# Performance work log

Measured on AMD Instinct MI355X. Metric: run time of the kernel, lower is better.

The kernel has to match this reference:

```python
import jax, jax.numpy as jnp
import numpy as np

L, H, D, N, M, P, C, IMG, B = 12, 12, 768, 197, 3072, 16, 3, 224, 16
SKIP_AT = (3, 6, 9, 12)


def pos_emb(n, d):
    i = jnp.arange(n, dtype=jnp.float32)[:, None]
    j = jnp.arange(d)[None, :]
    je = (j // 2) * 2  # j for even, j-1 for odd
    ang = i / jnp.power(10000.0, je.astype(jnp.float32) / d)
    return jnp.where(j % 2 == 0, jnp.sin(ang), jnp.cos(ang))  # [n, d]


def layer_norm(x, g, b):
    mu = x.mean(-1, keepdims=True)
    var = x.var(-1, keepdims=True)
    return (x - mu) / jnp.sqrt(var + 1e-5) * g + b


def setup_inputs() -> dict:
    key = jax.random.key(0)
    ks = jax.random.split(key, 16)
    s = 0.02
    f32 = jnp.float32
    return {
        "images": jax.random.normal(ks[0], (B, C, IMG, IMG), f32),
        "class_token": jax.random.uniform(ks[1], (1, D), f32),
        "Wp": jax.random.normal(ks[2], (D, P * P * C), f32) * s,
        "bp": jnp.zeros((D,), f32),
        "Wq": jax.random.normal(ks[3], (L, H, D, D), f32) * s,
        "bq": jnp.zeros((L, H, D), f32),
        "Wk": jax.random.normal(ks[4], (L, H, D, D), f32) * s,
        "bk": jnp.zeros((L, H, D), f32),
        "Wv": jax.random.normal(ks[5], (L, H, D, D), f32) * s,
        "bv": jnp.zeros((L, H, D), f32),
        "Wm": jax.random.normal(ks[6], (L, N, H * N), f32) * s,
        "bm": jnp.zeros((L, N), f32),
        "g1": jnp.ones((L, D), f32),
        "be1": jnp.zeros((L, D), f32),
        "W1": jax.random.normal(ks[7], (L, M, D), f32) * s,
        "b1": jnp.zeros((L, M), f32),
        "W2": jax.random.normal(ks[8], (L, D, M), f32) * s,
        "b2": jnp.zeros((L, D), f32),
        "g2": jnp.ones((L, D), f32),
        "be2": jnp.zeros((L, D), f32),
    }


def reference(images, class_token, Wp, bp, Wq, bq, Wk, bk, Wv, bv, Wm, bm,
              g1, be1, W1, b1, W2, b2, g2, be2):
    b = images.shape[0]
    Hn, Wn = IMG // P, IMG // P
    # einops 'b c (patch_x h) (patch_y w) -> b (h w) (patch_x patch_y c)'
    x = images.reshape(b, C, P, Hn, P, Wn).transpose(0, 3, 5, 2, 4, 1)
    patches = x.reshape(b, Hn * Wn, P * P * C)
    tokens = patches @ Wp.T + bp  # [b, N-1, D]
    cls = jnp.broadcast_to(class_token[None], (b, 1, D))
    out = jnp.concatenate([cls, tokens], axis=1) + pos_emb(N, D)[None]
    scale = 1.0 / jnp.sqrt(jnp.float32(N - 1))
    skips = []
    for l in range(L):
        x0 = out
        q = jnp.einsum('bnd,hed->bhne', x0, Wq[l]) + bq[l][None, :, None, :]
        k = jnp.einsum('bnd,hed->bhne', x0, Wk[l]) + bk[l][None, :, None, :]
        v = jnp.einsum('bnd,hed->bhne', x0, Wv[l]) + bv[l][None, :, None, :]
        attn = jax.nn.softmax(jnp.einsum('bhne,bhme->bhnm', q, k) * scale, axis=-1)
        o = jnp.einsum('bhnm,bhme->bhne', attn, v).reshape(b, H * N, D)
        # transpose -> [b, D, H*N], Linear(H*N -> N), transpose back
        msa = jnp.einsum('bfd,nf->bnd', o, Wm[l]) + bm[l][None, :, None]
        x1 = layer_norm(x0 + msa, g1[l], be1[l])
        hdn = jax.nn.gelu(x1 @ W1[l].T + b1[l], approximate=False)
        out = layer_norm(x1 + (hdn @ W2[l].T + b2[l]), g2[l], be2[l])
        if l + 1 in SKIP_AT:
            skips.append(out[:, 1:, :])
    return (out[:, 1:, :], *skips)
```

## Files before the change

### kernel.cpp

```cpp
#include <hip/hip_runtime.h>
#include <cstdint>
#include <cstddef>

typedef __bf16 bf16;
typedef __bf16 bf16x8 __attribute__((ext_vector_type(8)));
typedef float f32x4 __attribute__((ext_vector_type(4)));

#define DEVINL __device__ __forceinline__

typedef const __attribute__((address_space(1))) void* as1cv;
typedef __attribute__((address_space(3))) void* as3v;

DEVINL void gload16(const bf16* g, bf16* l) {
    __builtin_amdgcn_global_load_lds((as1cv)g, (as3v)l, 16, 0, 0);
}

static constexpr int Lh = 12, Hh = 12, Dh = 768, Nh = 197, Mh = 3072, Bh = 16;
static constexpr int BN   = Bh * Nh;
static constexpr int NPAT = Bh * 196;
static constexpr int HD   = Hh * Dh;
static constexpr int QKN  = 2 * HD;
static constexpr int QKV3 = 3 * HD;
static constexpr int NP   = 256;
static constexpr int FHN  = Hh * Nh;
static constexpr int FP   = 2368;
static constexpr size_t SEC = (size_t)Bh * 196 * Dh;
static constexpr long LS3 = (long)QKV3 * Dh;
static constexpr long PART = (long)BN * Dh;

template<int AF32, int BF32, int OUTBF, int BIAS, int ACT, int ZFILL>
__global__ __launch_bounds__(256, 3) void gemm_bt(
    const void* __restrict__ Av, long sAy, long sAz, int lda,
    const void* __restrict__ Bv, long sBy, long sBz, int ldb,
    void* __restrict__ Cv, long sCy, long sCz, int ldc,
    const float* __restrict__ bias, long sBiasY,
    int Mv, int Nv, int K, int tilesN, int kChunk)
{
    __shared__ __align__(16) bf16 Asm[128 * 32];
    __shared__ __align__(16) bf16 Bsm[128 * 32];
    const int bx = blockIdx.x;
    const int tm = bx / tilesN, tn = bx % tilesN;
    const long aoff = (long)blockIdx.y * sAy + (long)blockIdx.z * sAz + (long)tm * 128 * lda;
    const long boff = (long)blockIdx.y * sBy + (long)blockIdx.z * sBz + (long)tn * 128 * ldb;
    const int tid = threadIdx.x;
    const int lane = tid & 63, wid = tid >> 6;
    const int ar = tid >> 2, ac = (tid & 3) << 3;
    const bf16* Ag = (const bf16*)Av + aoff + (long)ar * lda + ac;
    const bf16* Bg = (const bf16*)Bv + boff + (long)ar * ldb + ac;
    const float* Af = (const float*)Av + aoff + (long)ar * lda + ac;
    const float* Bf = (const float*)Bv + boff + (long)ar * ldb + ac;
    bf16* lA = Asm + wid * 512;
    bf16* lB = Bsm + wid * 512;
    const int mw = (wid >> 1) * 64, nw = (wid & 1) * 64;
    const int fr = lane & 15, fq = lane >> 4;
    const int kBeg = kChunk ? blockIdx.y * kChunk : 0;
    const int kEnd = kChunk ? min(K, kBeg + kChunk) : K;
    f32x4 acc[4][4] = {};
    for (int k0 = kBeg; k0 < kEnd; k0 += 32) {
        if (AF32) {
            const float* p0 = Af + k0;
            const float* p1 = p0 + (long)64 * lda;
            f32x4 a0 = *(const f32x4*)p0, a1 = *(const f32x4*)(p0 + 4);
            f32x4 a2 = *(const f32x4*)p1, a3 = *(const f32x4*)(p1 + 4);
            bf16x8 r0, r1;
#pragma unroll
            for (int i = 0; i < 4; i++) { r0[i] = (bf16)a0[i]; r0[i + 4] = (bf16)a1[i];
                                          r1[i] = (bf16)a2[i]; r1[i + 4] = (bf16)a3[i]; }
            *(bf16x8*)&Asm[ar * 32 + ac] = r0;
            *(bf16x8*)&Asm[(ar + 64) * 32 + ac] = r1;
        } else {
            gload16(Ag + k0, lA);
            gload16(Ag + (long)64 * lda + k0, lA + 2048);
        }
        if (BF32) {
            const float* p0 = Bf + k0;
            const float* p1 = p0 + (long)64 * ldb;
            f32x4 a0 = *(const f32x4*)p0, a1 = *(const f32x4*)(p0 + 4);
            f32x4 a2 = *(const f32x4*)p1, a3 = *(const f32x4*)(p1 + 4);
            bf16x8 r0, r1;
#pragma unroll
            for (int i = 0; i < 4; i++) { r0[i] = (bf16)a0[i]; r0[i + 4] = (bf16)a1[i];
                                          r1[i] = (bf16)a2[i]; r1[i + 4] = (bf16)a3[i]; }
            *(bf16x8*)&Bsm[ar * 32 + ac] = r0;
            *(bf16x8*)&Bsm[(ar + 64) * 32 + ac] = r1;
        } else {
            gload16(Bg + k0, lB);
            gload16(Bg + (long)64 * ldb + k0, lB + 2048);
        }
        __syncthreads();
        bf16x8 af[4], bv[4];
#pragma unroll
        for (int i = 0; i < 4; i++) af[i] = *(const bf16x8*)&Asm[(mw + i * 16 + fr) * 32 + (fq << 3)];
#pragma unroll
        for (int j = 0; j < 4; j++) bv[j] = *(const bf16x8*)&Bsm[(nw + j * 16 + fr) * 32 + (fq << 3)];
#pragma unroll
        for (int i = 0; i < 4; i++)
#pragma unroll
            for (int j = 0; j < 4; j++)
                acc[i][j] = __builtin_amdgcn_mfma_f32_16x16x32_bf16(af[i], bv[j], acc[i][j], 0, 0, 0);
        __syncthreads();
    }
    const long cb = (long)blockIdx.y * sCy + (long)blockIdx.z * sCz;
    const float* biasp = bias ? bias + (long)blockIdx.y * sBiasY : nullptr;
#pragma unroll
    for (int i = 0; i < 4; i++) {
        const int row0 = tm * 128 + mw + i * 16 + fq * 4;
#pragma unroll
        for (int j = 0; j < 4; j++) {
            const int col = tn * 128 + nw + j * 16 + fr;
            const bool cok = (col < Nv);
            if (!cok && !ZFILL) continue;
            float bc = (BIAS == 1 && cok) ? biasp[col] : 0.f;
#pragma unroll
            for (int r = 0; r < 4; r++) {
                const int rr = row0 + r;
                if (rr >= Mv) continue;
                float v;
                if (cok) {
                    v = acc[i][j][r];
                    if (BIAS == 1) v += bc;
                    if (BIAS == 2) v += biasp[rr];
                    if (ACT) v = 0.5f * v * (1.f + erff(v * 0.70710678118654752f));
                } else v = 0.f;
                const long ci = cb + (long)rr * ldc + col;
                if (OUTBF) ((bf16*)Cv)[ci] = (bf16)v;
                else       ((float*)Cv)[ci] = v;
            }
        }
    }
}

__global__ __launch_bounds__(512, 2) void gemm256(
    const bf16* __restrict__ A, int lda,
    const bf16* __restrict__ B, int ldb,
    bf16* __restrict__ C, int ldc,
    const float* __restrict__ bias,
    int Mv, int K, int tilesN)
{
    __shared__ __align__(16) bf16 As[2][2][8192];
    __shared__ __align__(16) bf16 Bs[2][2][8192];
    const int bx = blockIdx.x;
    const int bm = (bx / tilesN) * 256, bn = (bx % tilesN) * 256;
    const int tid = threadIdx.x;
    const int lane = tid & 63, wid = tid >> 6;
    const int wr = wid >> 2, wc = wid & 3;
    const int fr = lane & 15, fq = lane >> 4;
    const int srow = lane >> 3;
    const int scol = (((lane & 7) ^ srow) << 3);
    const int KT = K >> 6;

    auto STA = [&](int buf, int half, int kt) {
        const bf16* g = A + (size_t)(bm + half * 128) * lda + kt * 64 + scol;
        bf16* l0 = &As[buf][half][0] + wid * 512;
#pragma unroll
        for (int j = 0; j < 2; ++j)
            gload16(g + (size_t)(wid * 8 + j * 64 + srow) * lda, l0 + j * 4096);
    };
    auto STB = [&](int buf, int half, int kt) {
        const bf16* g = B + (size_t)(bn + half * 128) * ldb + kt * 64 + scol;
        bf16* l0 = &Bs[buf][half][0] + wid * 512;
#pragma unroll
        for (int j = 0; j < 2; ++j)
            gload16(g + (size_t)(wid * 8 + j * 64 + srow) * ldb, l0 + j * 4096);
    };

    f32x4 acc[8][4] = {};
    const int swz = (fr & 7) << 3;

    STB(0, 0, 0); STB(0, 1, 0);
    STA(0, 0, 0); STA(0, 1, 0);
    if (KT > 1) { STB(1, 0, 1); STB(1, 1, 1); }
    if (KT > 1) asm volatile("s_waitcnt vmcnt(4)" ::: "memory");
    else        asm volatile("s_waitcnt vmcnt(0)" ::: "memory");
    asm volatile("s_barrier" ::: "memory");

    for (int t = 0; t < KT; ++t) {
        const int d = t & 1;
        bf16x8 bfr[4][2];
#pragma unroll
        for (int q = 0; q < 4; ++q) {
            if (q == 0) {
#pragma unroll
                for (int j = 0; j < 4; ++j)
#pragma unroll
                    for (int ks = 0; ks < 2; ++ks) {
                        const int rl = (wc & 1) * 64 + j * 16 + fr;
                        bfr[j][ks] = *(const bf16x8*)&Bs[d][wc >> 1][rl * 64 + (((ks << 5) | (fq << 3)) ^ swz)];
                    }
            }
            bf16x8 afr[2][2];
#pragma unroll
            for (int ii = 0; ii < 2; ++ii)
#pragma unroll
                for (int ks = 0; ks < 2; ++ks) {
                    const int rl = q * 32 + ii * 16 + fr;
                    afr[ii][ks] = *(const bf16x8*)&As[d][wr][rl * 64 + (((ks << 5) | (fq << 3)) ^ swz)];
                }
            if (q == 0 && t + 1 < KT) STA(d ^ 1, 0, t + 1);
            if (q == 1 && t + 1 < KT) STA(d ^ 1, 1, t + 1);
            if (q == 2 && t + 2 < KT) STB(d, 0, t + 2);
            if (q == 3 && t + 2 < KT) STB(d, 1, t + 2);
            asm volatile("s_barrier" ::: "memory");
            asm volatile("s_waitcnt lgkmcnt(0)" ::: "memory");
            __builtin_amdgcn_s_setprio(1);
#pragma unroll
            for (int ks = 0; ks < 2; ++ks)
#pragma unroll
                for (int ii = 0; ii < 2; ++ii)
#pragma unroll
                    for (int j = 0; j < 4; ++j)
                        acc[(q << 1) | ii][j] =
                            __builtin_amdgcn_mfma_f32_16x16x32_bf16(afr[ii][ks], bfr[j][ks],
                                                                    acc[(q << 1) | ii][j], 0, 0, 0);
            __builtin_amdgcn_s_setprio(0);
            if (q == 3) {
                if (t + 2 < KT) asm volatile("s_waitcnt vmcnt(4)" ::: "memory");
                else            asm volatile("s_waitcnt vmcnt(0)" ::: "memory");
            }
            asm volatile("s_barrier" ::: "memory");
        }
    }

    const int row0c = bm + wr * 128;
    const int col0 = bn + wc * 64;
#pragma unroll
    for (int ri = 0; ri < 8; ++ri)
#pragma unroll
        for (int j = 0; j < 4; ++j) {
            const int col = col0 + j * 16 + fr;
            const float bc = bias[col];
#pragma unroll
            for (int r = 0; r < 4; ++r) {
                const int rr = row0c + ri * 16 + fq * 4 + r;
                if (rr < Mv) C[(size_t)rr * ldc + col] = (bf16)(acc[ri][j][r] + bc);
            }
        }
}

__global__ __launch_bounds__(256) void vtrans_k(const bf16* __restrict__ qkv, bf16* __restrict__ vT) {
    __shared__ bf16 t[64][72];
    const int eb = (blockIdx.x >> 2) << 6;
    const int nb = (blockIdx.x & 3) << 6;
    const int h = blockIdx.y, b = blockIdx.z;
    const int tid = threadIdx.x;
    const int lr = tid >> 2;
    const int lc = (tid & 3) << 4;
    const int n = nb + lr;
    if (n < Nh) {
        const bf16* src = qkv + (size_t)(b * Nh + n) * QKV3 + 2 * HD + h * Dh + eb + lc;
        *(bf16x8*)&t[lr][lc] = *(const bf16x8*)src;
        *(bf16x8*)&t[lr][lc + 8] = *(const bf16x8*)(src + 8);
    } else {
        bf16x8 z = {};
        *(bf16x8*)&t[lr][lc] = z; *(bf16x8*)&t[lr][lc + 8] = z;
    }
    __syncthreads();
    bf16* dst = vT + ((size_t)(b * Hh + h) * Dh + eb + lr) * NP + nb + lc;
    bf16x8 o0, o1;
#pragma unroll
    for (int j = 0; j < 8; j++) { o0[j] = t[lc + j][lr]; o1[j] = t[lc + 8 + j][lr]; }
    *(bf16x8*)dst = o0; *(bf16x8*)(dst + 8) = o1;
}

__global__ __launch_bounds__(256) void cvt_k(const float* __restrict__ in, bf16* __restrict__ out, long n) {
    const long i = ((long)blockIdx.x * 256 + threadIdx.x) * 8;
    if (i >= n) return;
    f32x4 a = *(const f32x4*)(in + i);
    f32x4 b = *(const f32x4*)(in + i + 4);
    bf16x8 r;
#pragma unroll
    for (int j = 0; j < 4; j++) { r[j] = (bf16)a[j]; r[j + 4] = (bf16)b[j]; }
    *(bf16x8*)(out + i) = r;
}

__global__ __launch_bounds__(256) void cvt_s_k(const float* __restrict__ in, bf16* __restrict__ out,
                                               long perLayer, long dstStride, long dstOff, long total) {
    const long i = ((long)blockIdx.x * 256 + threadIdx.x) * 8;
    if (i >= total) return;
    const long l = i / perLayer, r = i % perLayer;
    f32x4 a = *(const f32x4*)(in + i);
    f32x4 b = *(const f32x4*)(in + i + 4);
    bf16x8 v;
#pragma unroll
    for (int j = 0; j < 4; j++) { v[j] = (bf16)a[j]; v[j + 4] = (bf16)b[j]; }
    *(bf16x8*)(out + l * dstStride + dstOff + r) = v;
}

__global__ void qkvbias_k(const float* __restrict__ bq, const float* __restrict__ bk,
                          const float* __restrict__ bv, float* __restrict__ dst) {
    const int idx = blockIdx.x * 256 + threadIdx.x;
    if (idx >= Lh * QKV3) return;
    const int l = idx / QKV3, c = idx % QKV3;
    float v;
    if (c < HD) v = bq[l * HD + c];
    else if (c < 2 * HD) v = bk[l * HD + c - HD];
    else v = bv[l * HD + c - 2 * HD];
    dst[idx] = v;
}

__global__ void patch_k(const float* __restrict__ images, bf16* __restrict__ patches) {
    const long idx = (long)blockIdx.x * 256 + threadIdx.x;
    if (idx >= (long)NPAT * Dh) return;
    const int r = (int)(idx / Dh), f = (int)(idx % Dh);
    const int b = r / 196, pi = r % 196, h = pi / 14, w = pi % 14;
    const int px = f / 48, rem = f % 48, py = rem / 3, c = rem % 3;
    patches[idx] = (bf16)images[(((long)(b * 3 + c) * 224) + px * 14 + h) * 224 + py * 14 + w];
}

__global__ void assemble_k(const float* __restrict__ tokens, const float* __restrict__ cls,
                           float* __restrict__ x, bf16* __restrict__ xbf) {
    const long idx = (long)blockIdx.x * 256 + threadIdx.x;
    if (idx >= (long)BN * Dh) return;
    const int r = (int)(idx / Dh), d = (int)(idx % Dh);
    const int b = r / Nh, n = r % Nh;
    const int je = d & ~1;
    const float ang = (float)n / powf(10000.f, (float)je / 768.f);
    const float pe = (d & 1) ? cosf(ang) : sinf(ang);
    const float val = (n == 0) ? (cls[d] + pe)
                               : (tokens[((long)b * 196 + (n - 1)) * Dh + d] + pe);
    x[idx] = val;
    xbf[idx] = (bf16)val;
}

__global__ void wmpad_k(const float* __restrict__ Wm, bf16* __restrict__ WmP) {
    const long idx = (long)blockIdx.x * 256 + threadIdx.x;
    if (idx >= (long)Lh * 256 * FP) return;
    const int l = (int)(idx / (256 * FP));
    const int rem = (int)(idx % (256 * FP));
    const int n = rem / FP, f = rem % FP;
    bf16 v = (bf16)0.f;
    if (n < Nh && f < FHN) v = (bf16)Wm[((long)l * Nh + n) * FHN + f];
    WmP[idx] = v;
}

__global__ void otpad_k(bf16* __restrict__ oT, int cb) {
    const int idx = blockIdx.x * 256 + threadIdx.x;
    if (idx >= cb * Dh * 4) return;
    const int b = idx / (Dh * 4), rem = idx % (Dh * 4), e = rem / 4, f = rem % 4;
    oT[((long)b * Dh + e) * FP + FHN + f] = (bf16)0.f;
}

__global__ __launch_bounds__(256) void softmax_k(const float* __restrict__ S, bf16* __restrict__ P) {
    const int tid = threadIdx.x, lane = tid & 63, wv = tid >> 6;
    const long rr = (long)blockIdx.x * 4 + wv;
    const int bh = (int)(rr / Nh), n = (int)(rr % Nh);
    const float* s = S + ((long)bh * Nh + n) * NP;
    bf16* p = P + ((long)bh * NP + n) * NP;
    float v[4]; float mx = -1e30f;
#pragma unroll
    for (int i = 0; i < 4; i++) {
        const int c = lane + i * 64;
        const float t = (c < Nh) ? s[c] * (1.f / 14.f) : -1e30f;
        v[i] = t; mx = fmaxf(mx, t);
    }
    for (int o = 32; o; o >>= 1) mx = fmaxf(mx, __shfl_xor(mx, o));
    float sum = 0.f;
#pragma unroll
    for (int i = 0; i < 4; i++) {
        const int c = lane + i * 64;
        v[i] = (c < Nh) ? expf(v[i] - mx) : 0.f;
        sum += v[i];
    }
    for (int o = 32; o; o >>= 1) sum += __shfl_xor(sum, o);
    const float inv = 1.f / sum;
#pragma unroll
    for (int i = 0; i < 4; i++) p[lane + i * 64] = (bf16)(v[i] * inv);
}

template<int BIAS_ROW, int NPART>
__global__ __launch_bounds__(256) void add_ln_k(
    const float* __restrict__ in1, const float* __restrict__ in2, long pstride,
    const float* __restrict__ bias, const float* __restrict__ gamma, const float* __restrict__ beta,
    float* __restrict__ outF, bf16* __restrict__ outBF,
    float* __restrict__ dst0, float* __restrict__ dst1)
{
    const int r = blockIdx.x;
    const int b = r / Nh, n = r % Nh;
    const long base = (long)r * Dh;
    const int tid = threadIdx.x;
    const float rowb = BIAS_ROW ? bias[n] : 0.f;
    float v[3]; float s = 0.f, s2 = 0.f;
#pragma unroll
    for (int i = 0; i < 3; i++) {
        const int d = tid + 256 * i;
        float t = in1[base + d] + (BIAS_ROW ? rowb : bias[d]);
#pragma unroll
        for (int pp = 0; pp < NPART; pp++) t += in2[pp * pstride + base + d];
        v[i] = t; s += t; s2 += t * t;
    }
    for (int o = 32; o; o >>= 1) { s += __shfl_xor(s, o); s2 += __shfl_xor(s2, o); }
    __shared__ float red[8];
    const int lane = tid & 63, wv = tid >> 6;
    if (lane == 0) { red[wv] = s; red[4 + wv] = s2; }
    __syncthreads();
    s  = red[0] + red[1] + red[2] + red[3];
    s2 = red[4] + red[5] + red[6] + red[7];
    const float mu = s * (1.f / 768.f);
    const float var = s2 * (1.f / 768.f) - mu * mu;
    const float rs = rsqrtf(var + 1e-5f);
    const long ob = ((long)b * 196 + (n - 1)) * Dh;
#pragma unroll
    for (int i = 0; i < 3; i++) {
        const int d = tid + 256 * i;
        const float y = (v[i] - mu) * rs * gamma[d] + beta[d];
        outF[base + d] = y;
        outBF[base + d] = (bf16)y;
        if (n > 0) {
            if (dst0) dst0[ob + d] = y;
            if (dst1) dst1[ob + d] = y;
        }
    }
}

static inline size_t al256(size_t x) { return (x + 255) & ~(size_t)255; }

extern "C" void kernel_launch(void* const* d_in, const int* in_sizes, int n_in,
                              void* d_out, int out_size, void* d_ws, size_t ws_size,
                              hipStream_t stream) {
    (void)in_sizes; (void)n_in; (void)out_size;
    const float* images = (const float*)d_in[0];
    const float* cls    = (const float*)d_in[1];
    const float* Wp     = (const float*)d_in[2];
    const float* bp     = (const float*)d_in[3];
    const float* Wq     = (const float*)d_in[4];
    const float* bq     = (const float*)d_in[5];
    const float* Wk     = (const float*)d_in[6];
    const float* bk     = (const float*)d_in[7];
    const float* Wv     = (const float*)d_in[8];
    const float* bv     = (const float*)d_in[9];
    const float* Wm     = (const float*)d_in[10];
    const float* bm     = (const float*)d_in[11];
    const float* g1     = (const float*)d_in[12];
    const float* be1    = (const float*)d_in[13];
    const float* W1     = (const float*)d_in[14];
    const float* b1     = (const float*)d_in[15];
    const float* W2     = (const float*)d_in[16];
    const float* b2     = (const float*)d_in[17];
    const float* g2     = (const float*)d_in[18];
    const float* be2    = (const float*)d_in[19];
    float* out = (float*)d_out;

    const size_t xB    = al256(3152ull * 768 * 4);
    const size_t xbfB  = al256(3328ull * 768 * 2);
    const size_t x1B   = al256(3152ull * 768 * 4);
    const size_t x1bfB = al256(3200ull * 768 * 2);
    const size_t msaB  = al256(2ull * PART * 4);
    const size_t mlp2B = al256(4ull * PART * 4);
    const size_t wmpB  = al256(12ull * 256 * FP * 2);
    const size_t biasB = al256((size_t)Lh * QKV3 * 4);
    const size_t persistB = xB + xbfB + x1B + x1bfB + msaB + mlp2B + wmpB + biasB;
    const size_t hdnB  = al256(3200ull * 3072 * 2);
    const size_t preB  = al256(3200ull * 768 * 2) + al256(3136ull * 768 * 4);
    const size_t wqkvB = al256((size_t)Lh * HD * Dh * 2);
    const size_t w12B  = al256((size_t)Lh * Mh * Dh * 2);
    const size_t wpB   = al256(768ull * 768 * 2);
    const size_t weightsB = 3 * wqkvB + 2 * w12B + wpB;

    const size_t qkvbB = al256(3328ull * QKV3 * 2);
    const size_t vtB2  = al256((size_t)Bh * Hh * Dh * NP * 2);
    const size_t sB2   = al256((size_t)Bh * Hh * Nh * NP * 4);
    const size_t pB2   = al256((size_t)Bh * Hh * NP * NP * 2);
    const size_t otB2  = al256((size_t)Bh * Dh * FP * 2);
    size_t chunk2 = qkvbB + vtB2 + sB2 + pB2 + otB2;
    if (chunk2 < hdnB) chunk2 = hdnB;
    if (chunk2 < preB) chunk2 = preB;
    const size_t margin = (size_t)(8u << 20);
    const bool fusedV2 = (chunk2 + persistB + weightsB + margin <= ws_size);

    auto chunk_bytes = [&](int cb, size_t& qbB_o, size_t& vtB_o, size_t& sB_o) -> size_t {
        const size_t qbRows = (size_t)((cb * 197 + 127) / 128 + 1) * 128;
        size_t qbB = al256(qbRows * HD * 2);
        size_t vtB = al256((size_t)cb * Hh * Dh * NP * 2);
        size_t sB  = al256((size_t)cb * Hh * Nh * NP * 4);
        size_t c = 2 * qbB + vtB + sB;
        if (c < hdnB) c = hdnB;
        if (c < preB) c = preB;
        qbB_o = qbB; vtB_o = vtB; sB_o = sB;
        return c;
    };
    int CB = 16; bool useCvt = true;
    size_t qbB, vtB, sB, chunkB;
    if (fusedV2) {
        chunkB = chunk2; qbB = vtB = sB = 0;
    } else {
        for (;;) {
            chunkB = chunk_bytes(CB, qbB, vtB, sB);
            if (chunkB + persistB + weightsB + margin <= ws_size) break;
            if (CB == 1) { useCvt = false; break; }
            CB >>= 1;
        }
        if (!useCvt) {
            CB = 16;
            for (;;) {
                chunkB = chunk_bytes(CB, qbB, vtB, sB);
                if (chunkB + persistB + margin <= ws_size || CB == 1) break;
                CB >>= 1;
            }
        }
    }

    char* wsb = (char*)d_ws;
    bf16*  qkvb = (bf16*)wsb;
    bf16*  vT2  = (bf16*)(wsb + qkvbB);
    float* S2   = (float*)(wsb + qkvbB + vtB2);
    bf16*  P2   = (bf16*)(wsb + qkvbB + vtB2 + sB2);
    bf16*  oT2  = (bf16*)(wsb + qkvbB + vtB2 + sB2 + pB2);
    bf16*  qb  = (bf16*)wsb;
    bf16*  kb  = (bf16*)(wsb + qbB);
    bf16*  vT  = (bf16*)(wsb + 2 * qbB);
    float* S   = (float*)(wsb + 2 * qbB + vtB);
    bf16*  oT  = qb;
    bf16*  P   = kb;
    bf16*  hdn = (bf16*)wsb;
    bf16*  patches = (bf16*)wsb;
    float* tokens  = (float*)(wsb + al256(3200ull * 768 * 2));
    char* p = wsb + chunkB;
    float* x    = (float*)p; p += xB;
    bf16*  xbf  = (bf16*) p; p += xbfB;
    float* x1   = (float*)p; p += x1B;
    bf16*  x1bf = (bf16*) p; p += x1bfB;
    float* msaP = (float*)p; p += msaB;
    float* mlp2P= (float*)p; p += mlp2B;
    bf16*  WmP  = (bf16*) p; p += wmpB;
    float* qkvbias = (float*)p; p += biasB;
    bf16 *WqkvB = nullptr, *W1B = nullptr, *W2B = nullptr, *WpB = nullptr;
    const bool cvt = fusedV2 || useCvt;
    if (cvt) {
        WqkvB = (bf16*)p; p += 3 * wqkvB;
        W1B  = (bf16*)p; p += w12B;
        W2B  = (bf16*)p; p += w12B;
        WpB  = (bf16*)p; p += wpB;
    }

    if (cvt) {
        const long nqkv = (long)Lh * HD * Dh;
        const long n12  = (long)Lh * Mh * Dh;
        const int gq = (int)((nqkv / 8 + 255) / 256);
        const int g12 = (int)((n12 / 8 + 255) / 256);
        cvt_s_k<<<gq, 256, 0, stream>>>(Wq, WqkvB, (long)HD * Dh, LS3, 0, nqkv);
        cvt_s_k<<<gq, 256, 0, stream>>>(Wk, WqkvB, (long)HD * Dh, LS3, (long)HD * Dh, nqkv);
        cvt_s_k<<<gq, 256, 0, stream>>>(Wv, WqkvB, (long)HD * Dh, LS3, 2L * HD * Dh, nqkv);
        cvt_k<<<g12, 256, 0, stream>>>(W1, W1B, n12);
        cvt_k<<<g12, 256, 0, stream>>>(W2, W2B, n12);
        cvt_k<<<(768 * 768 / 8 + 255) / 256, 256, 0, stream>>>(Wp, WpB, 768 * 768);
        qkvbias_k<<<(Lh * QKV3 + 255) / 256, 256, 0, stream>>>(bq, bk, bv, qkvbias);
    }

    patch_k<<<9408, 256, 0, stream>>>(images, patches);
    if (cvt)
        gemm_bt<0, 0, 0, 1, 0, 0><<<dim3(25 * 6), 256, 0, stream>>>(
            patches, 0, 0, 768, WpB, 0, 0, 768, tokens, 0, 0, 768, bp, 0, NPAT, 768, 768, 6, 0);
    else
        gemm_bt<0, 1, 0, 1, 0, 0><<<dim3(25 * 6), 256, 0, stream>>>(
            patches, 0, 0, 768, Wp, 0, 0, 768, tokens, 0, 0, 768, bp, 0, NPAT, 768, 768, 6, 0);
    assemble_k<<<9456, 256, 0, stream>>>(tokens, cls, x, xbf);
    wmpad_k<<<28416, 256, 0, stream>>>(Wm, WmP);

    const int NCH = 16 / CB;
    const int tilesQ = (CB * 197 + 127) / 128;

    for (int l = 0; l < 12; l++) {
        const float* Wq_l = Wq + (size_t)l * HD * Dh;
        const float* Wk_l = Wk + (size_t)l * HD * Dh;
        const float* Wv_l = Wv + (size_t)l * HD * Dh;
        const bf16* Wqkv_l = cvt ? WqkvB + (size_t)l * LS3 : nullptr;
        const bf16* WqB_l = Wqkv_l;
        const bf16* WkB_l = cvt ? Wqkv_l + (size_t)HD * Dh : nullptr;
        const bf16* WvB_l = cvt ? Wqkv_l + 2 * (size_t)HD * Dh : nullptr;
        const float* bq_l = bq + (size_t)l * HD;
        const float* bk_l = bk + (size_t)l * HD;
        const float* bv_l = bv + (size_t)l * HD;
        const bf16*  WmP_l = WmP + (size_t)l * 256 * FP;
        const float* bm_l = bm + (size_t)l * Nh;
        const float* g1_l = g1 + (size_t)l * Dh;  const float* be1_l = be1 + (size_t)l * Dh;
        const float* W1_l = W1 + (size_t)l * Mh * Dh; const float* b1_l = b1 + (size_t)l * Mh;
        const float* W2_l = W2 + (size_t)l * Dh * Mh; const float* b2_l = b2 + (size_t)l * Dh;
        const bf16* W1B_l = cvt ? W1B + (size_t)l * Mh * Dh : nullptr;
        const bf16* W2B_l = cvt ? W2B + (size_t)l * Mh * Dh : nullptr;
        const float* g2_l = g2 + (size_t)l * Dh;  const float* be2_l = be2 + (size_t)l * Dh;

        if (fusedV2) {
            gemm256<<<dim3(13 * 108), 512, 0, stream>>>(
                xbf, 768, Wqkv_l, 768, qkvb, QKV3, qkvbias + (size_t)l * QKV3, BN, 768, 108);
            vtrans_k<<<dim3(48, 12, 16), 256, 0, stream>>>(qkvb, vT2);
            gemm_bt<0, 0, 0, 0, 0, 0><<<dim3(4, 12, 16), 256, 0, stream>>>(
                qkvb, 768, (long)Nh * QKV3, QKV3,
                qkvb + HD, 768, (long)Nh * QKV3, QKV3,
                S2, (long)Nh * NP, (long)Hh * Nh * NP, NP,
                nullptr, 0, Nh, Nh, 768, 2, 0);
            softmax_k<<<16 * 591, 256, 0, stream>>>(S2, P2);
            otpad_k<<<16 * 12, 256, 0, stream>>>(oT2, 16);
            gemm_bt<0, 0, 1, 0, 0, 0><<<dim3(12, 12, 16), 256, 0, stream>>>(
                vT2, (long)Dh * NP, (long)Hh * Dh * NP, NP,
                P2, (long)NP * NP, (long)Hh * NP * NP, NP,
                oT2, (long)Nh, (long)Dh * FP, FP,
                nullptr, 0, Dh, Nh, NP, 2, 0);
            gemm_bt<0, 0, 0, 0, 0, 0><<<dim3(12, 2, 16), 256, 0, stream>>>(
                WmP_l, 0, 0, FP,
                oT2, 0, (long)Dh * FP, FP,
                msaP, PART, (long)Nh * Dh, Dh,
                nullptr, 0, Nh, Dh, FP, 6, 1184);
        } else {
            for (int c = 0; c < NCH; c++) {
                const size_t r0 = (size_t)c * CB * Nh;
                if (useCvt) {
                    gemm_bt<0, 0, 1, 1, 0, 0><<<dim3(tilesQ * 72), 256, 0, stream>>>(
                        xbf + r0 * Dh, 0, 0, 768, WqB_l, 0, 0, 768, qb, 0, 0, HD, bq_l, 0, CB * Nh, HD, 768, 72, 0);
                    gemm_bt<0, 0, 1, 1, 0, 0><<<dim3(tilesQ * 72), 256, 0, stream>>>(
                        xbf + r0 * Dh, 0, 0, 768, WkB_l, 0, 0, 768, kb, 0, 0, HD, bk_l, 0, CB * Nh, HD, 768, 72, 0);
                    gemm_bt<0, 0, 1, 2, 0, 1><<<dim3(12, 12, CB), 256, 0, stream>>>(
                        WvB_l, (long)Dh * Dh, 0, 768,
                        xbf + r0 * Dh, 0, (long)Nh * Dh, 768,
                        vT, (long)Dh * NP, (long)Hh * Dh * NP, NP,
                        bv_l, Dh, 768, Nh, 768, 2, 0);
                } else {
                    gemm_bt<0, 1, 1, 1, 0, 0><<<dim3(tilesQ * 72), 256, 0, stream>>>(
                        xbf + r0 * Dh, 0, 0, 768, Wq_l, 0, 0, 768, qb, 0, 0, HD, bq_l, 0, CB * Nh, HD, 768, 72, 0);
                    gemm_bt<0, 1, 1, 1, 0, 0><<<dim3(tilesQ * 72), 256, 0, stream>>>(
                        xbf + r0 * Dh, 0, 0, 768, Wk_l, 0, 0, 768, kb, 0, 0, HD, bk_l, 0, CB * Nh, HD, 768, 72, 0);
                    gemm_bt<1, 0, 1, 2, 0, 1><<<dim3(12, 12, CB), 256, 0, stream>>>(
                        Wv_l, (long)Dh * Dh, 0, 768,
                        xbf + r0 * Dh, 0, (long)Nh * Dh, 768,
                        vT, (long)Dh * NP, (long)Hh * Dh * NP, NP,
                        bv_l, Dh, 768, Nh, 768, 2, 0);
                }
                gemm_bt<0, 0, 0, 0, 0, 0><<<dim3(4, 12, CB), 256, 0, stream>>>(
                    qb, Dh, (long)Nh * HD, HD,
                    kb, Dh, (long)Nh * HD, HD,
                    S, (long)Nh * NP, (long)Hh * Nh * NP, NP,
                    nullptr, 0, Nh, Nh, 768, 2, 0);
                softmax_k<<<CB * 591, 256, 0, stream>>>(S, P);
                otpad_k<<<CB * 12, 256, 0, stream>>>(oT, CB);
                gemm_bt<0, 0, 1, 0, 0, 0><<<dim3(12, 12, CB), 256, 0, stream>>>(
                    vT, (long)Dh * NP, (long)Hh * Dh * NP, NP,
                    P, (long)NP * NP, (long)Hh * NP * NP, NP,
                    oT, (long)Nh, (long)Dh * FP, FP,
                    nullptr, 0, Dh, Nh, NP, 2, 0);
                gemm_bt<0, 0, 0, 0, 0, 0><<<dim3(12, 2, CB), 256, 0, stream>>>(
                    WmP_l, 0, 0, FP,
                    oT, 0, (long)Dh * FP, FP,
                    msaP + r0 * Dh, PART, (long)Nh * Dh, Dh,
                    nullptr, 0, Nh, Dh, FP, 6, 1184);
            }
        }
        add_ln_k<1, 2><<<BN, 256, 0, stream>>>(x, msaP, PART, bm_l, g1_l, be1_l, x1, x1bf, nullptr, nullptr);
        if (cvt) {
            gemm_bt<0, 0, 1, 1, 1, 0><<<dim3(25 * 24), 256, 0, stream>>>(
                x1bf, 0, 0, 768, W1B_l, 0, 0, 768, hdn, 0, 0, Mh, b1_l, 0, BN, Mh, 768, 24, 0);
            gemm_bt<0, 0, 0, 0, 0, 0><<<dim3(25 * 6, 4, 1), 256, 0, stream>>>(
                hdn, 0, 0, Mh, W2B_l, 0, 0, Mh, mlp2P, PART, 0, Dh, nullptr, 0, BN, Dh, Mh, 6, 768);
        } else {
            gemm_bt<0, 1, 1, 1, 1, 0><<<dim3(25 * 24), 256, 0, stream>>>(
                x1bf, 0, 0, 768, W1_l, 0, 0, 768, hdn, 0, 0, Mh, b1_l, 0, BN, Mh, 768, 24, 0);
            gemm_bt<0, 1, 0, 0, 0, 0><<<dim3(25 * 6, 4, 1), 256, 0, stream>>>(
                hdn, 0, 0, Mh, W2_l, 0, 0, Mh, mlp2P, PART, 0, Dh, nullptr, 0, BN, Dh, Mh, 6, 768);
        }
        float* d0 = nullptr; float* d1 = nullptr;
        if (l == 2)  d0 = out + 1 * SEC;
        if (l == 5)  d0 = out + 2 * SEC;
        if (l == 8)  d0 = out + 3 * SEC;
        if (l == 11) { d0 = out; d1 = out + 4 * SEC; }
        add_ln_k<0, 4><<<BN, 256, 0, stream>>>(x1, mlp2P, PART, b2_l, g2_l, be2_l, x, xbf, d0, d1);
    }
}
```

Measured before the change: 6.833 ms.

## Fuse V transpose into QKV GEMM epilogue and remap workgroups across XCDs

The QKV GEMM now writes the V third of its output directly in transposed [b,h,e,n] layout, which removes the separate vtrans kernel and the round trip of V through the qkv buffer. Q/K are stored with a narrower row stride. Workgroup IDs are remapped so consecutive tiles land on the same XCD, with M-major tile ordering to improve L2 reuse of weight tiles. The vT zero padding and the oT padding now run once up front instead of every layer. The transposed V stores are scattered 2-byte writes with poor coalescing, which may offset the saved kernel.

Result: slower. 7.475 ms (+9.4%).

```diff
diff --git a/kernel.cpp b/kernel.cpp
--- a/kernel.cpp
+++ b/kernel.cpp
@@ -133,14 +133,19 @@
 __global__ __launch_bounds__(512, 2) void gemm256(
     const bf16* __restrict__ A, int lda,
     const bf16* __restrict__ B, int ldb,
-    bf16* __restrict__ C, int ldc,
+    bf16* __restrict__ C,
     const float* __restrict__ bias,
-    int Mv, int K, int tilesN)
+    bf16* __restrict__ vT,
+    int Mv, int K, int tilesM)
 {
     __shared__ __align__(16) bf16 As[2][2][8192];
     __shared__ __align__(16) bf16 Bs[2][2][8192];
-    const int bx = blockIdx.x;
-    const int bm = (bx / tilesN) * 256, bn = (bx % tilesN) * 256;
+    const int nwg = gridDim.x;
+    const int xcd = blockIdx.x & 7, idx = blockIdx.x >> 3;
+    const int q8 = nwg >> 3, r8 = nwg & 7;
+    const int wgid = (xcd < r8 ? xcd * (q8 + 1) : r8 * (q8 + 1) + (xcd - r8) * q8) + idx;
+    const int tm = wgid % tilesM, tn = wgid / tilesM;
+    const int bm = tm * 256, bn = tn * 256;
     const int tid = threadIdx.x;
     const int lane = tid & 63, wid = tid >> 6;
     const int wr = wid >> 2, wc = wid & 3;
@@ -223,43 +228,38 @@
 
     const int row0c = bm + wr * 128;
     const int col0 = bn + wc * 64;
-#pragma unroll
-    for (int ri = 0; ri < 8; ++ri)
-#pragma unroll
-        for (int j = 0; j < 4; ++j) {
-            const int col = col0 + j * 16 + fr;
-            const float bc = bias[col];
-#pragma unroll
-            for (int r = 0; r < 4; ++r) {
-                const int rr = row0c + ri * 16 + fq * 4 + r;
-                if (rr < Mv) C[(size_t)rr * ldc + col] = (bf16)(acc[ri][j][r] + bc);
+    if (bn < QKN) {
+#pragma unroll
+        for (int ri = 0; ri < 8; ++ri)
+#pragma unroll
+            for (int j = 0; j < 4; ++j) {
+                const int col = col0 + j * 16 + fr;
+                const float bc = bias[col];
+#pragma unroll
+                for (int r = 0; r < 4; ++r) {
+                    const int rr = row0c + ri * 16 + fq * 4 + r;
+                    if (rr < Mv) C[(size_t)rr * QKN + col] = (bf16)(acc[ri][j][r] + bc);
+                }
             }
-        }
-}
-
-__global__ __launch_bounds__(256) void vtrans_k(const bf16* __restrict__ qkv, bf16* __restrict__ vT) {
-    __shared__ bf16 t[64][72];
-    const int eb = (blockIdx.x >> 2) << 6;
-    const int nb = (blockIdx.x & 3) << 6;
-    const int h = blockIdx.y, b = blockIdx.z;
-    const int tid = threadIdx.x;
-    const int lr = tid >> 2;
-    const int lc = (tid & 3) << 4;
-    const int n = nb + lr;
-    if (n < Nh) {
-        const bf16* src = qkv + (size_t)(b * Nh + n) * QKV3 + 2 * HD + h * Dh + eb + lc;
-        *(bf16x8*)&t[lr][lc] = *(const bf16x8*)src;
-        *(bf16x8*)&t[lr][lc + 8] = *(const bf16x8*)(src + 8);
     } else {
-        bf16x8 z = {};
-        *(bf16x8*)&t[lr][lc] = z; *(bf16x8*)&t[lr][lc + 8] = z;
-    }
-    __syncthreads();
-    bf16* dst = vT + ((size_t)(b * Hh + h) * Dh + eb + lr) * NP + nb + lc;
-    bf16x8 o0, o1;
-#pragma unroll
-    for (int j = 0; j < 8; j++) { o0[j] = t[lc + j][lr]; o1[j] = t[lc + 8 + j][lr]; }
-    *(bf16x8*)dst = o0; *(bf16x8*)(dst + 8) = o1;
+#pragma unroll
+        for (int ri = 0; ri < 8; ++ri)
+#pragma unroll
+            for (int j = 0; j < 4; ++j) {
+                const int col = col0 + j * 16 + fr;
+                const float bc = bias[col];
+                const int vcol = col - QKN;
+                const int h = vcol / Dh, e = vcol % Dh;
+#pragma unroll
+                for (int r = 0; r < 4; ++r) {
+                    const int rr = row0c + ri * 16 + fq * 4 + r;
+                    if (rr < Mv) {
+                        const int b = rr / Nh, n = rr % Nh;
+                        vT[((size_t)(b * Hh + h) * Dh + e) * NP + n] = (bf16)(acc[ri][j][r] + bc);
+                    }
+                }
+            }
+    }
 }
 
 __global__ __launch_bounds__(256) void cvt_k(const float* __restrict__ in, bf16* __restrict__ out, long n) {
@@ -456,7 +456,7 @@
     const size_t wpB   = al256(768ull * 768 * 2);
     const size_t weightsB = 3 * wqkvB + 2 * w12B + wpB;
 
-    const size_t qkvbB = al256(3328ull * QKV3 * 2);
+    const size_t qkvbB = al256(3328ull * QKN * 2);
     const size_t vtB2  = al256((size_t)Bh * Hh * Dh * NP * 2);
     const size_t sB2   = al256((size_t)Bh * Hh * Nh * NP * 4);
     const size_t pB2   = al256((size_t)Bh * Hh * NP * NP * 2);
@@ -555,6 +555,10 @@
             patches, 0, 0, 768, Wp, 0, 0, 768, tokens, 0, 0, 768, bp, 0, NPAT, 768, 768, 6, 0);
     assemble_k<<<9456, 256, 0, stream>>>(tokens, cls, x, xbf);
     wmpad_k<<<28416, 256, 0, stream>>>(Wm, WmP);
+    if (fusedV2) {
+        hipMemsetAsync(vT2, 0, vtB2, stream);
+        otpad_k<<<16 * 12, 256, 0, stream>>>(oT2, 16);
+    }
 
     const int NCH = 16 / CB;
     const int tilesQ = (CB * 197 + 127) / 128;
@@ -581,15 +585,13 @@
 
         if (fusedV2) {
             gemm256<<<dim3(13 * 108), 512, 0, stream>>>(
-                xbf, 768, Wqkv_l, 768, qkvb, QKV3, qkvbias + (size_t)l * QKV3, BN, 768, 108);
-            vtrans_k<<<dim3(48, 12, 16), 256, 0, stream>>>(qkvb, vT2);
+                xbf, 768, Wqkv_l, 768, qkvb, qkvbias + (size_t)l * QKV3, vT2, BN, 768, 13);
             gemm_bt<0, 0, 0, 0, 0, 0><<<dim3(4, 12, 16), 256, 0, stream>>>(
-                qkvb, 768, (long)Nh * QKV3, QKV3,
-                qkvb + HD, 768, (long)Nh * QKV3, QKV3,
+                qkvb, 768, (long)Nh * QKN, QKN,
+                qkvb + HD, 768, (long)Nh * QKN, QKN,
                 S2, (long)Nh * NP, (long)Hh * Nh * NP, NP,
                 nullptr, 0, Nh, Nh, 768, 2, 0);
             softmax_k<<<16 * 591, 256, 0, stream>>>(S2, P2);
-            otpad_k<<<16 * 12, 256, 0, stream>>>(oT2, 16);
             gemm_bt<0, 0, 1, 0, 0, 0><<<dim3(12, 12, 16), 256, 0, stream>>>(
                 vT2, (long)Dh * NP, (long)Hh * Dh * NP, NP,
                 P2, (long)NP * NP, (long)Hh * NP * NP, NP,
```
